# Kernel tuning notes

Measured on AMD Instinct MI355X. Metric: run time of the kernel, lower is better.

## Reference

```python
import jax, jax.numpy as jnp
import numpy as np

N = 100000      # nodes
E = 1600000     # edges (avg degree 16)
IN = 128
OUT = 256


def setup_inputs() -> dict:
    key = jax.random.key(0)
    ks = jax.random.split(key, 8)
    x = jax.random.normal(ks[0], (N, IN), dtype=jnp.float32)
    edge_index = jax.random.randint(ks[1], (2, E), 0, N, dtype=jnp.int64)
    # GCNConv weights (glorot-ish scale) and biases
    W1 = jax.random.normal(ks[2], (IN, OUT), dtype=jnp.float32) / np.float32(np.sqrt(IN))
    b1 = jnp.zeros((OUT,), jnp.float32)
    W2 = jax.random.normal(ks[3], (OUT, OUT), dtype=jnp.float32) / np.float32(np.sqrt(OUT))
    b2 = jnp.zeros((OUT,), jnp.float32)
    # projection Linear(IN, OUT)
    Wp = jax.random.normal(ks[4], (IN, OUT), dtype=jnp.float32) / np.float32(np.sqrt(IN))
    bp = jax.random.normal(ks[5], (OUT,), dtype=jnp.float32) * 0.01
    return {"x": x, "edge_index": edge_index, "W1": W1, "b1": b1,
            "W2": W2, "b2": b2, "Wp": Wp, "bp": bp}


def _gcn_conv(x, W, b, src, dst, n):
    """PyG GCNConv: D^{-1/2}(A+I)D^{-1/2} X W + b. src/dst already include self-loops."""
    xw = x @ W                                              # [n, out]
    ones = jnp.ones(src.shape[0], dtype=xw.dtype)
    deg = jax.ops.segment_sum(ones, dst, num_segments=n)    # in-degree incl. self-loop
    dinv = jnp.where(deg > 0, jax.lax.rsqrt(deg), 0.0)
    norm = dinv[src] * dinv[dst]                            # [e]
    msgs = xw[src] * norm[:, None]                          # gather + scale
    out = jax.ops.segment_sum(msgs, dst, num_segments=n)    # scatter-add
    return out + b


def reference(x, edge_index, W1, b1, W2, b2, Wp, bp):
    n = x.shape[0]
    loop = jnp.arange(n, dtype=edge_index.dtype)            # self-loops
    src = jnp.concatenate([edge_index[0], loop])
    dst = jnp.concatenate([edge_index[1], loop])
    out = jax.nn.relu(_gcn_conv(x, W1, b1, src, dst, n))
    out = _gcn_conv(out, W2, b2, src, dst, n)
    identity = x @ Wp + bp                                  # projection (IN != OUT)
    return jax.nn.relu(out + identity)
```

## Files before the change

### kernel.cpp

```cpp
#include <hip/hip_runtime.h>

#define NODES 100000
#define EDGES 1600000
#define FIN   128
#define FOUT  256
#define NBUCK 196

typedef __bf16 bf16;
typedef __bf16 bf16x8 __attribute__((ext_vector_type(8)));
typedef __bf16 bf16x4 __attribute__((ext_vector_type(4)));
typedef __bf16 bf16x2 __attribute__((ext_vector_type(2)));
typedef float  f32x4  __attribute__((ext_vector_type(4)));
typedef float  f32x2  __attribute__((ext_vector_type(2)));

__device__ __forceinline__ f32x2 bf2f(unsigned w) {
    f32x2 r;
    r[0] = __uint_as_float(w << 16);
    r[1] = __uint_as_float(w & 0xffff0000u);
    return r;
}

__global__ __launch_bounds__(256) void detect_kernel(const void* __restrict__ x,
                                                     const int* __restrict__ ei,
                                                     int* __restrict__ flags) {
    __shared__ int s_f32_evidence;
    __shared__ int s_odd_nonzero;
    int t = threadIdx.x;
    if (t == 0) { s_f32_evidence = 0; s_odd_nonzero = 0; }
    __syncthreads();
    const bf16* xb = (const bf16*)x;
    int local_f32 = 0;
    for (int i = t; i < 4096; i += 256) {
        float v = fabsf((float)xb[i]);
        if (!(v < 1e4f)) local_f32 = 1;
    }
    if (local_f32) atomicOr(&s_f32_evidence, 1);
    int local_odd = 0;
    for (int k = t; k < 1024; k += 256) {
        if (ei[2 * k + 1] != 0) local_odd = 1;
    }
    if (local_odd) atomicOr(&s_odd_nonzero, 1);
    __syncthreads();
    if (t == 0) {
        flags[0] = s_f32_evidence ? 0 : 1;
        flags[1] = s_odd_nonzero ? 0 : 1;
    }
}

__device__ __forceinline__ int edge_at(const int* __restrict__ ei, int which, int i,
                                       int is64) {
    if (is64) return ei[2 * (which * EDGES + i)];
    return ei[which * EDGES + i];
}

__global__ __launch_bounds__(512) void deg_count(const int* __restrict__ ei,
                                                 int* __restrict__ deg,
                                                 int* __restrict__ bhist,
                                                 const int* __restrict__ flags) {
    __shared__ int lh[256];
    int t = threadIdx.x;
    if (t < 256) lh[t] = 0;
    __syncthreads();
    int i = blockIdx.x * 512 + t;
    if (i < EDGES) {
        int is64 = flags[1];
        int s = edge_at(ei, 0, i, is64);
        int d = edge_at(ei, 1, i, is64);
        if (s >= 0 && s < NODES && d >= 0 && d < NODES) {
            atomicAdd(&deg[d], 1);
            atomicAdd(&lh[d >> 9], 1);
        }
    }
    __syncthreads();
    if (t < NBUCK && lh[t] > 0) atomicAdd(&bhist[t], lh[t]);
}

__global__ __launch_bounds__(1024) void scan1(const int* __restrict__ deg,
                                              int* __restrict__ col_ptr,
                                              int* __restrict__ blksum, int n) {
    __shared__ int sm[1024];
    int t = threadIdx.x;
    int i = blockIdx.x * 1024 + t;
    int v = (i < n) ? deg[i] : 0;
    sm[t] = v;
    __syncthreads();
    for (int off = 1; off < 1024; off <<= 1) {
        int u = (t >= off) ? sm[t - off] : 0;
        __syncthreads();
        sm[t] += u;
        __syncthreads();
    }
    if (i <= n) col_ptr[i] = sm[t] - v;
    if (t == 1023) blksum[blockIdx.x] = sm[t];
}

__global__ __launch_bounds__(128) void scan2(int* blk, int nblk) {
    __shared__ int sm[128];
    int t = threadIdx.x;
    int v = (t < nblk) ? blk[t] : 0;
    sm[t] = v;
    __syncthreads();
    for (int off = 1; off < 128; off <<= 1) {
        int u = (t >= off) ? sm[t - off] : 0;
        __syncthreads();
        sm[t] += u;
        __syncthreads();
    }
    if (t < nblk) blk[t] = sm[t] - v;
}

__global__ __launch_bounds__(256) void scan3(int* __restrict__ col_ptr,
                                             const int* __restrict__ blkoff,
                                             const int* __restrict__ deg,
                                             float* __restrict__ dinv, int n) {
    int i = blockIdx.x * 256 + threadIdx.x;
    if (i <= n) col_ptr[i] += blkoff[i >> 10];
    if (i < n) dinv[i] = rsqrtf((float)deg[i] + 1.0f);
}

__global__ __launch_bounds__(256) void bucket_scan(const int* __restrict__ bhist,
                                                   int* __restrict__ bbase,
                                                   int* __restrict__ bcur) {
    __shared__ int sm[256];
    int t = threadIdx.x;
    int v = (t < NBUCK) ? bhist[t] : 0;
    sm[t] = v;
    __syncthreads();
    for (int off = 1; off < 256; off <<= 1) {
        int u = (t >= off) ? sm[t - off] : 0;
        __syncthreads();
        sm[t] += u;
        __syncthreads();
    }
    if (t < NBUCK) {
        int ex = sm[t] - v;
        bbase[t] = ex;
        bcur[t]  = ex;
        if (t == NBUCK - 1) bbase[NBUCK] = sm[t];
    }
}

#define EPB 4096
__global__ __launch_bounds__(256) void partition_edges(const int* __restrict__ ei,
                                                       int* __restrict__ bcur,
                                                       uint2* __restrict__ pairs,
                                                       const int* __restrict__ flags) {
    __shared__ int lh[256], sc[256], lst[256], lcu[256], gb[256];
    __shared__ uint2 stage[EPB];
    int t = threadIdx.x;
    int base = blockIdx.x * EPB;
    int is64 = flags[1];

    lh[t] = 0;
    __syncthreads();

    int es[16], ed[16];
#pragma unroll
    for (int j = 0; j < 16; ++j) {
        int i = base + j * 256 + t;
        int s = -1, d = -1;
        if (i < EDGES) {
            s = edge_at(ei, 0, i, is64);
            d = edge_at(ei, 1, i, is64);
            if (s < 0 || s >= NODES || d < 0 || d >= NODES) d = -1;
        }
        es[j] = s; ed[j] = d;
        if (d >= 0) atomicAdd(&lh[d >> 9], 1);
    }
    __syncthreads();
    sc[t] = lh[t];
    __syncthreads();
    for (int off = 1; off < 256; off <<= 1) {
        int u = (t >= off) ? sc[t - off] : 0;
        __syncthreads();
        sc[t] += u;
        __syncthreads();
    }
    int start = sc[t] - lh[t];
    lst[t] = start;
    lcu[t] = start;
    __syncthreads();
#pragma unroll
    for (int j = 0; j < 16; ++j) {
        if (ed[j] >= 0) {
            int p = atomicAdd(&lcu[ed[j] >> 9], 1);
            stage[p] = make_uint2((unsigned)es[j], (unsigned)ed[j]);
        }
    }
    __syncthreads();
    if (t < NBUCK && lh[t] > 0) gb[t] = atomicAdd(&bcur[t], lh[t]);
    __syncthreads();
    int nval = sc[255];
    for (int slot = t; slot < nval; slot += 256) {
        uint2 e = stage[slot];
        int b = (int)(e.y >> 9);
        pairs[(size_t)gb[b] + (slot - lst[b])] = e;
    }
}

__global__ __launch_bounds__(512) void fine_fill(const uint2* __restrict__ pairs,
                                                 const int* __restrict__ bbase,
                                                 const int* __restrict__ col_ptr,
                                                 int* __restrict__ col_idx) {
    __shared__ int lcur[512];
    int b = blockIdx.x;
    int t = threadIdx.x;
    int node = (b << 9) + t;
    lcur[t] = (node < NODES) ? col_ptr[node] : 0;
    __syncthreads();
    int beg = bbase[b], end = bbase[b + 1];
    for (int i = beg + t; i < end; i += 512) {
        uint2 e = pairs[i];
        int pos = atomicAdd(&lcur[e.y & 511], 1);
        col_idx[pos] = (int)e.x;
    }
}

__global__ __launch_bounds__(256) void pack_all(const void* __restrict__ W1,
                                                const void* __restrict__ W2,
                                                const void* __restrict__ Wp,
                                                const void* __restrict__ b1,
                                                const void* __restrict__ b2,
                                                const void* __restrict__ bp,
                                                bf16* __restrict__ W1p, bf16* __restrict__ W2p,
                                                bf16* __restrict__ Wpp, bf16* __restrict__ b1b,
                                                bf16* __restrict__ b2b, bf16* __restrict__ bpb,
                                                const int* __restrict__ flags) {
    int fl = flags[0];
    int b = blockIdx.x;
    if (b < 512) {
        const void* W; bf16* Wo; int idx;
        if (b < 128)      { W = W1; Wo = W1p; idx = b * 256 + threadIdx.x; }
        else if (b < 384) { W = W2; Wo = W2p; idx = (b - 128) * 256 + threadIdx.x; }
        else              { W = Wp; Wo = Wpp; idx = (b - 384) * 256 + threadIdx.x; }
        int j    = idx & 7;
        int lane = (idx >> 3) & 63;
        int ct   = (idx >> 9) & 15;
        int kt   = idx >> 13;
        int k = kt * 32 + (lane >> 4) * 8 + j;
        int n = ct * 16 + (lane & 15);
        Wo[idx] = fl ? ((const bf16*)W)[k * 256 + n]
                     : (bf16)(((const float*)W)[k * 256 + n]);
    } else {
        const void* bb; bf16* bo;
        if (b == 512)      { bb = b1; bo = b1b; }
        else if (b == 513) { bb = b2; bo = b2b; }
        else               { bb = bp; bo = bpb; }
        int i = threadIdx.x;
        bo[i] = fl ? ((const bf16*)bb)[i] : (bf16)(((const float*)bb)[i]);
    }
}

__global__ __launch_bounds__(256) void scale_x(const void* __restrict__ xv,
                                               const float* __restrict__ dinv,
                                               bf16* __restrict__ Xs,
                                               const int* __restrict__ flags) {
    int idx = blockIdx.x * 256 + threadIdx.x;
    if (idx >= NODES * 16) return;
    int row = idx >> 4, seg = idx & 15;
    float di = dinv[row];
    bf16x8 o;
    if (flags[0]) {
        bf16x8 v = *(const bf16x8*)((const bf16*)xv + (size_t)row * FIN + seg * 8);
#pragma unroll
        for (int j = 0; j < 8; ++j) o[j] = (bf16)(di * (float)v[j]);
    } else {
        const float* p = (const float*)xv + (size_t)row * FIN + seg * 8;
        f32x4 lo = *(const f32x4*)p;
        f32x4 hi = *(const f32x4*)(p + 4);
#pragma unroll
        for (int j = 0; j < 4; ++j) { o[j] = (bf16)(di * lo[j]); o[j + 4] = (bf16)(di * hi[j]); }
    }
    *(bf16x8*)(Xs + (size_t)row * FIN + seg * 8) = o;
}

__global__ __launch_bounds__(256) void gemm_proj(const void* __restrict__ Av,
                                                 const bf16* __restrict__ Wpk,
                                                 const bf16* __restrict__ biasp,
                                                 const bf16* __restrict__ bias2,
                                                 bf16* __restrict__ projb,
                                                 const int* __restrict__ flags) {
    int a_f32 = (flags[0] == 0);
    int wave = threadIdx.x >> 6;
    int lane = threadIdx.x & 63;
    int row0 = blockIdx.x * 64;
    int lr = lane & 15;
    int lk = (lane >> 4) * 8;

    int arow[4];
#pragma unroll
    for (int rf = 0; rf < 4; ++rf) {
        int r = row0 + rf * 16 + lr;
        arow[rf] = r < NODES ? r : (NODES - 1);
    }

    f32x4 acc[4][4];
    f32x4 z = {0.f, 0.f, 0.f, 0.f};
#pragma unroll
    for (int i = 0; i < 4; ++i)
#pragma unroll
        for (int j = 0; j < 4; ++j) acc[i][j] = z;

    for (int kt = 0; kt < 4; ++kt) {
        bf16x8 af[4];
        if (!a_f32) {
            const bf16* Ab = (const bf16*)Av + kt * 32 + lk;
#pragma unroll
            for (int rf = 0; rf < 4; ++rf)
                af[rf] = *(const bf16x8*)(Ab + (size_t)arow[rf] * FIN);
        } else {
            const float* Af = (const float*)Av + kt * 32 + lk;
#pragma unroll
            for (int rf = 0; rf < 4; ++rf) {
                const float* p = Af + (size_t)arow[rf] * FIN;
                f32x4 lo = *(const f32x4*)p;
                f32x4 hi = *(const f32x4*)(p + 4);
                af[rf][0] = (bf16)lo[0]; af[rf][1] = (bf16)lo[1];
                af[rf][2] = (bf16)lo[2]; af[rf][3] = (bf16)lo[3];
                af[rf][4] = (bf16)hi[0]; af[rf][5] = (bf16)hi[1];
                af[rf][6] = (bf16)hi[2]; af[rf][7] = (bf16)hi[3];
            }
        }
        const bf16* wb = Wpk + ((size_t)(kt * 16 + wave * 4) * 64 + lane) * 8;
        bf16x8 bfv[4];
#pragma unroll
        for (int cf = 0; cf < 4; ++cf)
            bfv[cf] = *(const bf16x8*)(wb + cf * 512);
#pragma unroll
        for (int rf = 0; rf < 4; ++rf)
#pragma unroll
            for (int cf = 0; cf < 4; ++cf)
                acc[rf][cf] = __builtin_amdgcn_mfma_f32_16x16x32_bf16(
                    af[rf], bfv[cf], acc[rf][cf], 0, 0, 0);
    }

    int rb = (lane >> 4) * 4;
#pragma unroll
    for (int rf = 0; rf < 4; ++rf) {
#pragma unroll
        for (int r = 0; r < 4; ++r) {
            int row = row0 + rf * 16 + rb + r;
            if (row >= NODES) continue;
#pragma unroll
            for (int cf = 0; cf < 4; ++cf) {
                int col = wave * 64 + cf * 16 + lr;
                float v = acc[rf][cf][r] + (float)biasp[col] + (float)bias2[col];
                projb[(size_t)row * 256 + col] = (bf16)v;
            }
        }
    }
}

__global__ __launch_bounds__(256) void gemm_tile(const bf16* __restrict__ A,
                                                 const bf16* __restrict__ Wpk,
                                                 int K,
                                                 const float* __restrict__ dinv,
                                                 const bf16* __restrict__ bias,
                                                 int relu,
                                                 bf16* __restrict__ out) {
    int wave = threadIdx.x >> 6;
    int lane = threadIdx.x & 63;
    int row0 = blockIdx.x * 64;
    int lr = lane & 15;
    int lk = (lane >> 4) * 8;

    int arow[4];
#pragma unroll
    for (int rf = 0; rf < 4; ++rf) {
        int r = row0 + rf * 16 + lr;
        arow[rf] = r < NODES ? r : (NODES - 1);
    }

    f32x4 acc[4][4];
    f32x4 z = {0.f, 0.f, 0.f, 0.f};
#pragma unroll
    for (int i = 0; i < 4; ++i)
#pragma unroll
        for (int j = 0; j < 4; ++j) acc[i][j] = z;

    int ktiles = K >> 5;
    for (int kt = 0; kt < ktiles; ++kt) {
        const bf16* Ab = A + kt * 32 + lk;
        bf16x8 af[4];
#pragma unroll
        for (int rf = 0; rf < 4; ++rf)
            af[rf] = *(const bf16x8*)(Ab + (size_t)arow[rf] * K);
        const bf16* wb = Wpk + ((size_t)(kt * 16 + wave * 4) * 64 + lane) * 8;
        bf16x8 bfv[4];
#pragma unroll
        for (int cf = 0; cf < 4; ++cf)
            bfv[cf] = *(const bf16x8*)(wb + cf * 512);
#pragma unroll
        for (int rf = 0; rf < 4; ++rf)
#pragma unroll
            for (int cf = 0; cf < 4; ++cf)
                acc[rf][cf] = __builtin_amdgcn_mfma_f32_16x16x32_bf16(
                    af[rf], bfv[cf], acc[rf][cf], 0, 0, 0);
    }

    int rb = (lane >> 4) * 4;
#pragma unroll
    for (int rf = 0; rf < 4; ++rf) {
#pragma unroll
        for (int r = 0; r < 4; ++r) {
            int row = row0 + rf * 16 + rb + r;
            if (row >= NODES) continue;
            float s = dinv ? dinv[row] : 1.0f;
#pragma unroll
            for (int cf = 0; cf < 4; ++cf) {
                int col = wave * 64 + cf * 16 + lr;
                float v = acc[rf][cf][r] * s;
                if (bias) v += (float)bias[col];
                if (relu) v = fmaxf(v, 0.0f);
                out[(size_t)row * 256 + col] = (bf16)v;
            }
        }
    }
}

__device__ __forceinline__ float sel_reduce8(f32x2 acc2[4], int rg) {
    f32x2 a  = (rg & 4) ? acc2[2] : acc2[0];
    f32x2 b  = (rg & 4) ? acc2[3] : acc2[1];
    f32x2 sa = (rg & 4) ? acc2[0] : acc2[2];
    f32x2 sb = (rg & 4) ? acc2[1] : acc2[3];
    f32x2 t;
    t[0] = __shfl_xor(sa[0], 32); t[1] = __shfl_xor(sa[1], 32); a += t;
    t[0] = __shfl_xor(sb[0], 32); t[1] = __shfl_xor(sb[1], 32); b += t;
    f32x2 c = (rg & 2) ? b : a;
    f32x2 s = (rg & 2) ? a : b;
    t[0] = __shfl_xor(s[0], 16); t[1] = __shfl_xor(s[1], 16); c += t;
    float e  = (rg & 1) ? c[1] : c[0];
    float s2 = (rg & 1) ? c[0] : c[1];
    e += __shfl_xor(s2, 8);
    return e;
}

__global__ __launch_bounds__(256) void gather1(const int* __restrict__ col_ptr,
                                               const int* __restrict__ col_idx,
                                               const bf16* __restrict__ Xs,
                                               const float* __restrict__ dinv,
                                               bf16* __restrict__ aggX) {
    int b = blockIdx.x;
    int slice = b & 1;
    int wave  = threadIdx.x >> 6;
    int wid   = (b >> 1) * 4 + wave;
    int lane  = threadIdx.x & 63;
    if (wid >= NODES) return;
    int beg = col_ptr[wid], end = col_ptr[wid + 1];
    int li = lane & 7;
    int rg = lane >> 3;
    int ch = slice * 64 + li * 8 + rg;

    float selfc = (float)Xs[(size_t)wid * FIN + ch];
    float di = dinv[wid];

    const char* Xl = (const char*)Xs + slice * 128 + li * 16;
    f32x2 acc2[4];
#pragma unroll
    for (int d = 0; d < 4; ++d) { acc2[d][0] = 0.f; acc2[d][1] = 0.f; }
    int npad = 0;
    for (int chunk = beg; chunk < end; chunk += 64) {
        int cnt = end - chunk;
        if (cnt > 64) cnt = 64;
        int padded = (cnt + 7) & ~7;
        npad += padded - cnt;
        int moff = ((lane < cnt) ? __builtin_nontemporal_load(col_idx + chunk + lane)
                                 : wid) << 8;
        int j = 0;
        for (; j + 16 <= padded; j += 16) {
            int so0 = __shfl(moff, j + rg);
            int so1 = __shfl(moff, j + 8 + rg);
            uint4 w0 = *(const uint4*)(Xl + (unsigned)so0);
            uint4 w1 = *(const uint4*)(Xl + (unsigned)so1);
            acc2[0] += bf2f(w0.x); acc2[1] += bf2f(w0.y);
            acc2[2] += bf2f(w0.z); acc2[3] += bf2f(w0.w);
            acc2[0] += bf2f(w1.x); acc2[1] += bf2f(w1.y);
            acc2[2] += bf2f(w1.z); acc2[3] += bf2f(w1.w);
        }
        for (; j < padded; j += 8) {
            int so = __shfl(moff, j + rg);
            uint4 w = *(const uint4*)(Xl + (unsigned)so);
            acc2[0] += bf2f(w.x); acc2[1] += bf2f(w.y);
            acc2[2] += bf2f(w.z); acc2[3] += bf2f(w.w);
        }
    }
    float aval = sel_reduce8(acc2, rg);

    float corr = (float)(1 - npad);
    float r = di * (aval + corr * selfc);
    aggX[(size_t)wid * FIN + ch] = (bf16)r;
}

__global__ __launch_bounds__(256) void gather2(const int* __restrict__ col_ptr,
                                               const int* __restrict__ col_idx,
                                               const bf16* __restrict__ Y2,
                                               const float* __restrict__ dinv,
                                               const bf16* __restrict__ projb,
                                               void* __restrict__ outv,
                                               const int* __restrict__ flags) {
    int io_f32 = (flags[0] == 0);
    int b = blockIdx.x;
    int slice = b & 3;
    int wave  = threadIdx.x >> 6;
    int wid   = (b >> 2) * 4 + wave;
    int lane  = threadIdx.x & 63;
    if (wid >= NODES) return;
    int beg = col_ptr[wid], end = col_ptr[wid + 1];
    int li = lane & 7;
    int rg = lane >> 3;
    int ch = slice * 64 + li * 8 + rg;
    size_t obase = (size_t)wid * 256 + ch;

    float selfc = (float)Y2[obase];
    float di = dinv[wid];
    float pj = (float)__builtin_nontemporal_load(projb + obase);

    const char* Yl = (const char*)Y2 + slice * 128 + li * 16;
    f32x2 acc2[4];
#pragma unroll
    for (int d = 0; d < 4; ++d) { acc2[d][0] = 0.f; acc2[d][1] = 0.f; }
    int npad = 0;
    for (int chunk = beg; chunk < end; chunk += 64) {
        int cnt = end - chunk;
        if (cnt > 64) cnt = 64;
        int padded = (cnt + 7) & ~7;
        npad += padded - cnt;
        int moff = ((lane < cnt) ? __builtin_nontemporal_load(col_idx + chunk + lane)
                                 : wid) << 9;
        int j = 0;
        for (; j + 16 <= padded; j += 16) {
            int so0 = __shfl(moff, j + rg);
            int so1 = __shfl(moff, j + 8 + rg);
            uint4 w0 = *(const uint4*)(Yl + (unsigned)so0);
            uint4 w1 = *(const uint4*)(Yl + (unsigned)so1);
            acc2[0] += bf2f(w0.x); acc2[1] += bf2f(w0.y);
            acc2[2] += bf2f(w0.z); acc2[3] += bf2f(w0.w);
            acc2[0] += bf2f(w1.x); acc2[1] += bf2f(w1.y);
            acc2[2] += bf2f(w1.z); acc2[3] += bf2f(w1.w);
        }
        for (; j < padded; j += 8) {
            int so = __shfl(moff, j + rg);
            uint4 w = *(const uint4*)(Yl + (unsigned)so);
            acc2[0] += bf2f(w.x); acc2[1] += bf2f(w.y);
            acc2[2] += bf2f(w.z); acc2[3] += bf2f(w.w);
        }
    }
    float aval = sel_reduce8(acc2, rg);

    float corr = (float)(1 - npad);
    float r = fmaxf(di * (aval + corr * selfc) + pj, 0.0f);

    if (io_f32) {
        __builtin_nontemporal_store(r, (float*)outv + obase);
    } else {
        __builtin_nontemporal_store((bf16)r, (bf16*)outv + obase);
    }
}

__global__ __launch_bounds__(256) void zero_out(bf16* out, int nelem) {
    int i = blockIdx.x * 256 + threadIdx.x;
    if (i < nelem) out[i] = (bf16)0.0f;
}

extern "C" void kernel_launch(void* const* d_in, const int* in_sizes, int n_in,
                              void* d_out, int out_size, void* d_ws, size_t ws_size,
                              hipStream_t stream) {
    const void* x   = d_in[0];
    const int*  ei  = (const int*)d_in[1];
    const void* W1  = d_in[2];
    const void* b1  = d_in[3];
    const void* W2  = d_in[4];
    const void* b2  = d_in[5];
    const void* Wp  = d_in[6];
    const void* bp  = d_in[7];

    const size_t NEEDED = 401408ull * 3 + 1024ull * 4 + 6400000 + 65536 + 131072 + 65536
                        + 1536 + 25600000ull * 2 + 51200000ull;
    if (ws_size < NEEDED) {
        zero_out<<<(NODES * 256 + 255) / 256, 256, 0, stream>>>((bf16*)d_out, NODES * 256);
        return;
    }

    char* w = (char*)d_ws;
    int*   col_ptr = (int*)w;   w += 401408;
    int*   deg     = (int*)w;   w += 401408;
    int*   bhist   = (int*)w;   w += 1024;
    float* dinv    = (float*)w; w += 401408;
    int*   blk     = (int*)w;   w += 1024;
    int*   flags   = (int*)w;   w += 1024;
    int*   bbase   = (int*)w;   w += 1024;
    int*   bcur    = (int*)w;   w += 1024;
    int*   col_idx = (int*)w;   w += 6400000;
    bf16*  W1p     = (bf16*)w;  w += 65536;
    bf16*  W2p     = (bf16*)w;  w += 131072;
    bf16*  Wpp     = (bf16*)w;  w += 65536;
    bf16*  b1b     = (bf16*)w;  w += 512;
    bf16*  b2b     = (bf16*)w;  w += 512;
    bf16*  bpb     = (bf16*)w;  w += 512;
    bf16*  Xs      = (bf16*)w;  w += 25600000;
    bf16*  aggX    = (bf16*)w;  w += 25600000;
    bf16*  H1      = (bf16*)w;  w += 51200000;
    uint2* pairs   = (uint2*)Xs;
    bf16*  Y2      = Xs;
    bf16*  projb   = H1;

    const int NBLK = (NODES + 1 + 1023) / 1024;

    detect_kernel<<<1, 256, 0, stream>>>(x, ei, flags);

    hipMemsetAsync(deg, 0, 401408 + 1024, stream);
    deg_count<<<(EDGES + 511) / 512, 512, 0, stream>>>(ei, deg, bhist, flags);

    scan1<<<NBLK, 1024, 0, stream>>>(deg, col_ptr, blk, NODES);
    scan2<<<1, 128, 0, stream>>>(blk, NBLK);
    scan3<<<(NODES + 256) / 256, 256, 0, stream>>>(col_ptr, blk, deg, dinv, NODES);
    bucket_scan<<<1, 256, 0, stream>>>(bhist, bbase, bcur);

    partition_edges<<<(EDGES + EPB - 1) / EPB, 256, 0, stream>>>(ei, bcur, pairs, flags);
    fine_fill<<<NBUCK, 512, 0, stream>>>(pairs, bbase, col_ptr, col_idx);

    pack_all<<<515, 256, 0, stream>>>(W1, W2, Wp, b1, b2, bp,
                                      W1p, W2p, Wpp, b1b, b2b, bpb, flags);

    const int gemm_grid = (NODES + 63) / 64;
    const int g1_grid   = ((NODES + 3) / 4) * 2;
    const int g2_grid   = ((NODES + 3) / 4) * 4;

    scale_x<<<(NODES * 16 + 255) / 256, 256, 0, stream>>>(x, dinv, Xs, flags);
    gather1<<<g1_grid, 256, 0, stream>>>(col_ptr, col_idx, Xs, dinv, aggX);
    gemm_tile<<<gemm_grid, 256, 0, stream>>>(aggX, W1p, FIN, nullptr, b1b, 1, H1);
    gemm_tile<<<gemm_grid, 256, 0, stream>>>(H1, W2p, FOUT, dinv, nullptr, 0, Y2);
    gemm_proj<<<gemm_grid, 256, 0, stream>>>(x, Wpp, bpb, b2b, projb, flags);
    gather2<<<g2_grid, 256, 0, stream>>>(col_ptr, col_idx, Y2, dinv,
                                         projb, d_out, flags);
}
```

Measured before the change: 672.2 us.

## Store self-loops in CSR and widen gather2 slices with zero-pad sentinel rows

The self-loop for each node is now written as the first entry of its CSR row, so the gather kernels no longer load a separate self value or track padding corrections. Tail lanes use index -2, which points into a zeroed pad region placed before Xs and Y2, so partial chunks read zeros instead of the node's own row. gather2 now covers 128 channels per slice with 16 lanes x 2 channel pairs and issues four loads per iteration. This halves its grid and lets it write the output in 2-element vector stores. In exchange the CSR grows by N entries and correctness depends on a negative offset landing in the zeroed pad.

```diff
diff --git a/kernel.cpp b/kernel.cpp
--- a/kernel.cpp
+++ b/kernel.cpp
@@ -18,6 +18,11 @@
     r[0] = __uint_as_float(w << 16);
     r[1] = __uint_as_float(w & 0xffff0000u);
     return r;
+}
+
+__device__ __forceinline__ void acc_u4(f32x2 a[4], uint4 w) {
+    a[0] += bf2f(w.x); a[1] += bf2f(w.y);
+    a[2] += bf2f(w.z); a[3] += bf2f(w.w);
 }
 
 __global__ __launch_bounds__(256) void detect_kernel(const void* __restrict__ x,
@@ -81,7 +86,7 @@
     __shared__ int sm[1024];
     int t = threadIdx.x;
     int i = blockIdx.x * 1024 + t;
-    int v = (i < n) ? deg[i] : 0;
+    int v = (i < n) ? deg[i] + 1 : 0;
     sm[t] = v;
     __syncthreads();
     for (int off = 1; off < 1024; off <<= 1) {
@@ -112,9 +117,14 @@
 __global__ __launch_bounds__(256) void scan3(int* __restrict__ col_ptr,
                                              const int* __restrict__ blkoff,
                                              const int* __restrict__ deg,
-                                             float* __restrict__ dinv, int n) {
+                                             float* __restrict__ dinv,
+                                             int* __restrict__ col_idx, int n) {
     int i = blockIdx.x * 256 + threadIdx.x;
-    if (i <= n) col_ptr[i] += blkoff[i >> 10];
+    if (i <= n) {
+        int v = col_ptr[i] + blkoff[i >> 10];
+        col_ptr[i] = v;
+        if (i < n) col_idx[v] = i;
+    }
     if (i < n) dinv[i] = rsqrtf((float)deg[i] + 1.0f);
 }
 
@@ -206,7 +216,7 @@
     int b = blockIdx.x;
     int t = threadIdx.x;
     int node = (b << 9) + t;
-    lcur[t] = (node < NODES) ? col_ptr[node] : 0;
+    lcur[t] = (node < NODES) ? col_ptr[node] + 1 : 0;
     __syncthreads();
     int beg = bbase[b], end = bbase[b + 1];
     for (int i = beg + t; i < end; i += 512) {
@@ -435,6 +445,20 @@
     return e;
 }
 
+__device__ __forceinline__ f32x2 sel_reduce4(f32x2 a[4], int rg) {
+    f32x2 k0 = (rg & 2) ? a[2] : a[0];
+    f32x2 k1 = (rg & 2) ? a[3] : a[1];
+    f32x2 s0 = (rg & 2) ? a[0] : a[2];
+    f32x2 s1 = (rg & 2) ? a[1] : a[3];
+    f32x2 t;
+    t[0] = __shfl_xor(s0[0], 32); t[1] = __shfl_xor(s0[1], 32); k0 += t;
+    t[0] = __shfl_xor(s1[0], 32); t[1] = __shfl_xor(s1[1], 32); k1 += t;
+    f32x2 c = (rg & 1) ? k1 : k0;
+    f32x2 s = (rg & 1) ? k0 : k1;
+    t[0] = __shfl_xor(s[0], 16); t[1] = __shfl_xor(s[1], 16); c += t;
+    return c;
+}
+
 __global__ __launch_bounds__(256) void gather1(const int* __restrict__ col_ptr,
                                                const int* __restrict__ col_idx,
                                                const bf16* __restrict__ Xs,
@@ -450,45 +474,34 @@
     int li = lane & 7;
     int rg = lane >> 3;
     int ch = slice * 64 + li * 8 + rg;
-
-    float selfc = (float)Xs[(size_t)wid * FIN + ch];
     float di = dinv[wid];
 
     const char* Xl = (const char*)Xs + slice * 128 + li * 16;
     f32x2 acc2[4];
 #pragma unroll
     for (int d = 0; d < 4; ++d) { acc2[d][0] = 0.f; acc2[d][1] = 0.f; }
-    int npad = 0;
     for (int chunk = beg; chunk < end; chunk += 64) {
-        int cnt = end - chunk;
-        if (cnt > 64) cnt = 64;
-        int padded = (cnt + 7) & ~7;
-        npad += padded - cnt;
-        int moff = ((lane < cnt) ? __builtin_nontemporal_load(col_idx + chunk + lane)
-                                 : wid) << 8;
+        int gpos = chunk + lane;
+        int idx = -2;
+        if (gpos < end) idx = col_idx[gpos];
+        int moff = idx << 8;
+        int cnt = end - chunk; if (cnt > 64) cnt = 64;
         int j = 0;
-        for (; j + 16 <= padded; j += 16) {
+        for (; j + 16 <= cnt; j += 16) {
             int so0 = __shfl(moff, j + rg);
             int so1 = __shfl(moff, j + 8 + rg);
-            uint4 w0 = *(const uint4*)(Xl + (unsigned)so0);
-            uint4 w1 = *(const uint4*)(Xl + (unsigned)so1);
-            acc2[0] += bf2f(w0.x); acc2[1] += bf2f(w0.y);
-            acc2[2] += bf2f(w0.z); acc2[3] += bf2f(w0.w);
-            acc2[0] += bf2f(w1.x); acc2[1] += bf2f(w1.y);
-            acc2[2] += bf2f(w1.z); acc2[3] += bf2f(w1.w);
-        }
-        for (; j < padded; j += 8) {
+            uint4 w0 = *(const uint4*)(Xl + so0);
+            uint4 w1 = *(const uint4*)(Xl + so1);
+            acc_u4(acc2, w0); acc_u4(acc2, w1);
+        }
+        for (; j < cnt; j += 8) {
             int so = __shfl(moff, j + rg);
-            uint4 w = *(const uint4*)(Xl + (unsigned)so);
-            acc2[0] += bf2f(w.x); acc2[1] += bf2f(w.y);
-            acc2[2] += bf2f(w.z); acc2[3] += bf2f(w.w);
+            uint4 w = *(const uint4*)(Xl + so);
+            acc_u4(acc2, w);
         }
     }
     float aval = sel_reduce8(acc2, rg);
-
-    float corr = (float)(1 - npad);
-    float r = di * (aval + corr * selfc);
-    aggX[(size_t)wid * FIN + ch] = (bf16)r;
+    aggX[(size_t)wid * FIN + ch] = (bf16)(di * aval);
 }
 
 __global__ __launch_bounds__(256) void gather2(const int* __restrict__ col_ptr,
@@ -500,60 +513,59 @@
                                                const int* __restrict__ flags) {
     int io_f32 = (flags[0] == 0);
     int b = blockIdx.x;
-    int slice = b & 3;
+    int slice = b & 1;
     int wave  = threadIdx.x >> 6;
-    int wid   = (b >> 2) * 4 + wave;
+    int wid   = (b >> 1) * 4 + wave;
     int lane  = threadIdx.x & 63;
     if (wid >= NODES) return;
     int beg = col_ptr[wid], end = col_ptr[wid + 1];
-    int li = lane & 7;
-    int rg = lane >> 3;
-    int ch = slice * 64 + li * 8 + rg;
-    size_t obase = (size_t)wid * 256 + ch;
-
-    float selfc = (float)Y2[obase];
+    int li = lane & 15;
+    int rg = lane >> 4;
+    int ch0 = slice * 128 + li * 8 + rg * 2;
+    size_t obase = (size_t)wid * 256 + ch0;
+
     float di = dinv[wid];
-    float pj = (float)__builtin_nontemporal_load(projb + obase);
-
-    const char* Yl = (const char*)Y2 + slice * 128 + li * 16;
+    bf16x2 pjv = *(const bf16x2*)(projb + obase);
+
+    const char* Yl = (const char*)Y2 + slice * 256 + li * 16;
     f32x2 acc2[4];
 #pragma unroll
     for (int d = 0; d < 4; ++d) { acc2[d][0] = 0.f; acc2[d][1] = 0.f; }
-    int npad = 0;
     for (int chunk = beg; chunk < end; chunk += 64) {
-        int cnt = end - chunk;
-        if (cnt > 64) cnt = 64;
-        int padded = (cnt + 7) & ~7;
-        npad += padded - cnt;
-        int moff = ((lane < cnt) ? __builtin_nontemporal_load(col_idx + chunk + lane)
-                                 : wid) << 9;
+        int gpos = chunk + lane;
+        int idx = -2;
+        if (gpos < end) idx = col_idx[gpos];
+        int moff = idx << 9;
+        int cnt = end - chunk; if (cnt > 64) cnt = 64;
         int j = 0;
-        for (; j + 16 <= padded; j += 16) {
+        for (; j + 16 <= cnt; j += 16) {
             int so0 = __shfl(moff, j + rg);
-            int so1 = __shfl(moff, j + 8 + rg);
-            uint4 w0 = *(const uint4*)(Yl + (unsigned)so0);
-            uint4 w1 = *(const uint4*)(Yl + (unsigned)so1);
-            acc2[0] += bf2f(w0.x); acc2[1] += bf2f(w0.y);
-            acc2[2] += bf2f(w0.z); acc2[3] += bf2f(w0.w);
-            acc2[0] += bf2f(w1.x); acc2[1] += bf2f(w1.y);
-            acc2[2] += bf2f(w1.z); acc2[3] += bf2f(w1.w);
-        }
-        for (; j < padded; j += 8) {
+            int so1 = __shfl(moff, j + 4 + rg);
+            int so2 = __shfl(moff, j + 8 + rg);
+            int so3 = __shfl(moff, j + 12 + rg);
+            uint4 w0 = *(const uint4*)(Yl + so0);
+            uint4 w1 = *(const uint4*)(Yl + so1);
+            uint4 w2 = *(const uint4*)(Yl + so2);
+            uint4 w3 = *(const uint4*)(Yl + so3);
+            acc_u4(acc2, w0); acc_u4(acc2, w1);
+            acc_u4(acc2, w2); acc_u4(acc2, w3);
+        }
+        for (; j < cnt; j += 4) {
             int so = __shfl(moff, j + rg);
-            uint4 w = *(const uint4*)(Yl + (unsigned)so);
-            acc2[0] += bf2f(w.x); acc2[1] += bf2f(w.y);
-            acc2[2] += bf2f(w.z); acc2[3] += bf2f(w.w);
-        }
-    }
-    float aval = sel_reduce8(acc2, rg);
-
-    float corr = (float)(1 - npad);
-    float r = fmaxf(di * (aval + corr * selfc) + pj, 0.0f);
+            uint4 w = *(const uint4*)(Yl + so);
+            acc_u4(acc2, w);
+        }
+    }
+    f32x2 s = sel_reduce4(acc2, rg);
+    float r0 = fmaxf(di * s[0] + (float)pjv[0], 0.0f);
+    float r1 = fmaxf(di * s[1] + (float)pjv[1], 0.0f);
 
     if (io_f32) {
-        __builtin_nontemporal_store(r, (float*)outv + obase);
+        f32x2 o; o[0] = r0; o[1] = r1;
+        __builtin_nontemporal_store(o, (f32x2*)((float*)outv + obase));
     } else {
-        __builtin_nontemporal_store((bf16)r, (bf16*)outv + obase);
+        bf16x2 o; o[0] = (bf16)r0; o[1] = (bf16)r1;
+        __builtin_nontemporal_store(o, (bf16x2*)((bf16*)outv + obase));
     }
 }
 
@@ -574,8 +586,9 @@
     const void* Wp  = d_in[6];
     const void* bp  = d_in[7];
 
-    const size_t NEEDED = 401408ull * 3 + 1024ull * 4 + 6400000 + 65536 + 131072 + 65536
-                        + 1536 + 25600000ull * 2 + 51200000ull;
+    const size_t CIDX_ALLOC = 6800384;
+    const size_t NEEDED = 401408ull * 3 + 1024ull * 4 + CIDX_ALLOC + 65536 + 131072 + 65536
+                        + 1536 + 1024 + 25600000ull * 2 + 51200000ull;
     if (ws_size < NEEDED) {
         zero_out<<<(NODES * 256 + 255) / 256, 256, 0, stream>>>((bf16*)d_out, NODES * 256);
         return;
@@ -590,13 +603,14 @@
     int*   flags   = (int*)w;   w += 1024;
     int*   bbase   = (int*)w;   w += 1024;
     int*   bcur    = (int*)w;   w += 1024;
-    int*   col_idx = (int*)w;   w += 6400000;
+    int*   col_idx = (int*)w;   w += CIDX_ALLOC;
     bf16*  W1p     = (bf16*)w;  w += 65536;
     bf16*  W2p     = (bf16*)w;  w += 131072;
     bf16*  Wpp     = (bf16*)w;  w += 65536;
     bf16*  b1b     = (bf16*)w;  w += 512;
     bf16*  b2b     = (bf16*)w;  w += 512;
     bf16*  bpb     = (bf16*)w;  w += 512;
+    char*  zpad    = w;         w += 1024;
     bf16*  Xs      = (bf16*)w;  w += 25600000;
     bf16*  aggX    = (bf16*)w;  w += 25600000;
     bf16*  H1      = (bf16*)w;  w += 51200000;
@@ -607,13 +621,14 @@
     const int NBLK = (NODES + 1 + 1023) / 1024;
 
     detect_kernel<<<1, 256, 0, stream>>>(x, ei, flags);
+    hipMemsetAsync(zpad, 0, 1024, stream);
 
     hipMemsetAsync(deg, 0, 401408 + 1024, stream);
     deg_count<<<(EDGES + 511) / 512, 512, 0, stream>>>(ei, deg, bhist, flags);
 
     scan1<<<NBLK, 1024, 0, stream>>>(deg, col_ptr, blk, NODES);
     scan2<<<1, 128, 0, stream>>>(blk, NBLK);
-    scan3<<<(NODES + 256) / 256, 256, 0, stream>>>(col_ptr, blk, deg, dinv, NODES);
+    scan3<<<(NODES + 256) / 256, 256, 0, stream>>>(col_ptr, blk, deg, dinv, col_idx, NODES);
     bucket_scan<<<1, 256, 0, stream>>>(bhist, bbase, bcur);
 
     partition_edges<<<(EDGES + EPB - 1) / EPB, 256, 0, stream>>>(ei, bcur, pairs, flags);
@@ -623,14 +638,13 @@
                                       W1p, W2p, Wpp, b1b, b2b, bpb, flags);
 
     const int gemm_grid = (NODES + 63) / 64;
-    const int g1_grid   = ((NODES + 3) / 4) * 2;
-    const int g2_grid   = ((NODES + 3) / 4) * 4;
+    const int g_grid    = ((NODES + 3) / 4) * 2;
 
     scale_x<<<(NODES * 16 + 255) / 256, 256, 0, stream>>>(x, dinv, Xs, flags);
-    gather1<<<g1_grid, 256, 0, stream>>>(col_ptr, col_idx, Xs, dinv, aggX);
+    gather1<<<g_grid, 256, 0, stream>>>(col_ptr, col_idx, Xs, dinv, aggX);
     gemm_tile<<<gemm_grid, 256, 0, stream>>>(aggX, W1p, FIN, nullptr, b1b, 1, H1);
     gemm_tile<<<gemm_grid, 256, 0, stream>>>(H1, W2p, FOUT, dinv, nullptr, 0, Y2);
     gemm_proj<<<gemm_grid, 256, 0, stream>>>(x, Wpp, bpb, b2b, projb, flags);
-    gather2<<<g2_grid, 256, 0, stream>>>(col_ptr, col_idx, Y2, dinv,
-                                         projb, d_out, flags);
-}
+    gather2<<<g_grid, 256, 0, stream>>>(col_ptr, col_idx, Y2, dinv,
+                                        projb, d_out, flags);
+}
```

After: 649.5 us. 3.4% less time.
